# Kernel tuning notes

Hardware: AMD Instinct MI355X
Metric: run time of the kernel (lower is better)

The kernel has to match this reference:

```python
import jax, jax.numpy as jnp
import numpy as np

D_MODEL = 1024
D_FF = 4096


def _layernorm(x, g, b, eps=1e-5):
    mu = jnp.mean(x, axis=-1, keepdims=True)
    var = jnp.var(x, axis=-1, keepdims=True)
    return (x - mu) * jax.lax.rsqrt(var + eps) * g + b


def setup_inputs() -> dict:
    key = jax.random.key(0)
    ks = jax.random.split(key, 16)
    d, f = D_MODEL, D_FF
    s = 1.0 / np.sqrt(d)
    inp = {
        'x': jax.random.normal(ks[0], (4, 2048, d), dtype=jnp.float32),
        'wq': jax.random.uniform(ks[1], (d, d), jnp.float32, -s, s),
        'bq': jax.random.uniform(ks[2], (d,), jnp.float32, -s, s),
        'wk': jax.random.uniform(ks[3], (d, d), jnp.float32, -s, s),
        'bk': jax.random.uniform(ks[4], (d,), jnp.float32, -s, s),
        'wv': jax.random.uniform(ks[5], (d, d), jnp.float32, -s, s),
        'bv': jax.random.uniform(ks[6], (d,), jnp.float32, -s, s),
        'wo': jax.random.uniform(ks[7], (d, d), jnp.float32, -s, s),
        'bo': jax.random.uniform(ks[8], (d,), jnp.float32, -s, s),
        'w1': jax.random.uniform(ks[9], (d, f), jnp.float32, -s, s),
        'b1': jax.random.uniform(ks[10], (f,), jnp.float32, -s, s),
        'w2': jax.random.uniform(ks[11], (f, d), jnp.float32, -1.0 / np.sqrt(f), 1.0 / np.sqrt(f)),
        'b2': jax.random.uniform(ks[12], (d,), jnp.float32, -1.0 / np.sqrt(f), 1.0 / np.sqrt(f)),
        'g1': jnp.ones((d,), jnp.float32),
        'be1': jnp.zeros((d,), jnp.float32),
        'g2': jnp.ones((d,), jnp.float32),
        'be2': jnp.zeros((d,), jnp.float32),
    }
    return inp


def reference(x, wq, bq, wk, bk, wv, bv, wo, bo, w1, b1, w2, b2, g1, be1, g2, be2):
    d_k = x.shape[-1]
    q = jnp.einsum('bsd,de->bse', x, wq) + bq
    k = jnp.einsum('bsd,de->bse', x, wk) + bk
    v = jnp.einsum('bsd,de->bse', x, wv) + bv
    # full-width attention (no head split in the original module)
    scores = jnp.einsum('bqd,bkd->bqk', q, k) / jnp.sqrt(jnp.float32(d_k))
    attn = jax.nn.softmax(scores, axis=-1)
    ctx = jnp.einsum('bqk,bkd->bqd', attn, v)
    attn_out = jnp.einsum('bsd,de->bse', ctx, wo) + bo
    x1 = _layernorm(x + attn_out, g1, be1)
    ff = jnp.einsum('bsf,fd->bsd', jax.nn.relu(jnp.einsum('bsd,df->bsf', x1, w1) + b1), w2) + b2
    return _layernorm(x1 + ff, g2, be2)
```

## Files before the change

### kernel.cpp

```cpp
#include <hip/hip_runtime.h>
#include <stdint.h>


using f32x4 = __attribute__((ext_vector_type(4))) float;
using s16x8 = __attribute__((ext_vector_type(8))) short;

__device__ __forceinline__ ushort f2b(float f) {
    union { float f; uint32_t u; } v; v.f = f;
    uint32_t u = v.u;
    return (ushort)((u + 0x7fffu + ((u >> 16) & 1u)) >> 16);
}
__device__ __forceinline__ float b2f(ushort b) {
    union { uint32_t u; float f; } v; v.u = ((uint32_t)b) << 16;
    return v.f;
}
__device__ __forceinline__ float to_f(float f) { return f; }
__device__ __forceinline__ float to_f(ushort b) { return b2f(b); }

__device__ __forceinline__ void async_ld16(const ushort* g, ushort* l) {
    __builtin_amdgcn_global_load_lds(
        (const __attribute__((address_space(1))) void*)g,
        (__attribute__((address_space(3))) void*)l,
        16, 0, 0);
}

#define WAITCNT_VM4 0x0F74
#define WAITCNT_VM0 0x0F70


__global__ __launch_bounds__(256) void cast_f2b4(const float* __restrict__ src,
                                                 ushort* __restrict__ dst,
                                                 long long n4) {
    long long i = (long long)blockIdx.x * 256 + threadIdx.x;
    if (i >= n4) return;
    float4 f = ((const float4*)src)[i];
    ushort4 o;
    o.x = f2b(f.x); o.y = f2b(f.y); o.z = f2b(f.z); o.w = f2b(f.w);
    ((ushort4*)dst)[i] = o;
}


template <typename T>
__global__ __launch_bounds__(256) void transpose_to_bf16(const T* __restrict__ src,
                                                         ushort* __restrict__ dst,
                                                         int R, int C, int srcLd,
                                                         long long ss, long long ds) {
    __shared__ float tile[32][33];
    src += (long long)blockIdx.z * ss;
    dst += (long long)blockIdx.z * ds;
    const int c0 = blockIdx.x * 32;
    const int r0 = blockIdx.y * 32;
    const int tx = threadIdx.x, ty = threadIdx.y;
#pragma unroll
    for (int i = 0; i < 4; i++) {
        int r = r0 + ty + i * 8;
        tile[ty + i * 8][tx] = to_f(src[(long long)r * srcLd + c0 + tx]);
    }
    __syncthreads();
#pragma unroll
    for (int i = 0; i < 4; i++) {
        int r = c0 + ty + i * 8;
        dst[(long long)r * R + r0 + tx] = f2b(tile[tx][ty + i * 8]);
    }
}


#define BM 128
#define BN 128
#define BKK 32
#define TILE_ELEMS (BM * BKK)

template <int OUT_BF16, int RELU, int HAS_BIAS>
__global__ __launch_bounds__(256) void gemm_bt(const ushort* __restrict__ A,
                                               const ushort* __restrict__ BT,
                                               void* __restrict__ Cp,
                                               const float* __restrict__ bias,
                                               int N, int K, int kChunks, float scale,
                                               int lda, int ldb, int ldc,
                                               long long sA, long long sB, long long sC,
                                               long long sK) {
    __shared__ ushort As[2 * TILE_ELEMS];
    __shared__ ushort Bs[2 * TILE_ELEMS];

    const int tid = threadIdx.x;
    const int kIdx = blockIdx.z % kChunks;
    const int bz = blockIdx.z / kChunks;
    const int kLen = K / kChunks;
    const int kOff = kIdx * kLen;
    const ushort* Ab = A + (long long)bz * sA;
    const ushort* Bb = BT + (long long)bz * sB;

    const int W = gridDim.x, H = gridDim.y;
    const int b = blockIdx.y * W + blockIdx.x;
    const int Hp = H >> 3;
    const int xcd = b & 7;
    const int s = b >> 3;
    const int tn = s / Hp;
    const int tm = xcd * Hp + (s % Hp);

    const int lane = tid & 63;
    const int wave = tid >> 6;
    const int wm = (wave >> 1) * 64;
    const int wn = (wave & 1) * 64;
    const int quad = lane >> 4;
    const int l16 = lane & 15;

    const int srow = wave * 32 + (lane >> 2);
    const int scol = (lane & 3) * 8;
    const ushort* AgL = Ab + (long long)(tm * BM + srow) * lda + scol + kOff;
    const ushort* BgL = Bb + (long long)(tn * BN + srow) * ldb + scol + kOff;
    ushort* AsL = As + wave * 1024;
    ushort* BsL = Bs + wave * 1024;
    const long long rstepA = (long long)16 * lda;
    const long long rstepB = (long long)16 * ldb;

    f32x4 acc[4][4];
#pragma unroll
    for (int i = 0; i < 4; i++)
#pragma unroll
        for (int j = 0; j < 4; j++) acc[i][j] = (f32x4){0.f, 0.f, 0.f, 0.f};

    {
        async_ld16(AgL, AsL);
        async_ld16(AgL + rstepA, AsL + 512);
        async_ld16(BgL, BsL);
        async_ld16(BgL + rstepB, BsL + 512);
    }

    int p = 0;
    for (int k0 = 0; k0 < kLen; k0 += BKK) {
        if (k0 + BKK < kLen) {
            const int q = p ^ 1;
            async_ld16(AgL + (k0 + BKK), AsL + q * TILE_ELEMS);
            async_ld16(AgL + rstepA + (k0 + BKK), AsL + q * TILE_ELEMS + 512);
            async_ld16(BgL + (k0 + BKK), BsL + q * TILE_ELEMS);
            async_ld16(BgL + rstepB + (k0 + BKK), BsL + q * TILE_ELEMS + 512);
            __builtin_amdgcn_s_waitcnt(WAITCNT_VM4);
        } else {
            __builtin_amdgcn_s_waitcnt(WAITCNT_VM0);
        }
        __builtin_amdgcn_s_barrier();

        const ushort* Asp = As + p * TILE_ELEMS;
        const ushort* Bsp = Bs + p * TILE_ELEMS;
        s16x8 af[4], bf[4];
#pragma unroll
        for (int i = 0; i < 4; i++)
            af[i] = *(const s16x8*)&Asp[(wm + i * 16 + l16) * BKK + quad * 8];
#pragma unroll
        for (int j = 0; j < 4; j++)
            bf[j] = *(const s16x8*)&Bsp[(wn + j * 16 + l16) * BKK + quad * 8];
#pragma unroll
        for (int i = 0; i < 4; i++)
#pragma unroll
            for (int j = 0; j < 4; j++)
                acc[i][j] = __builtin_amdgcn_mfma_f32_16x16x32_bf16(af[i], bf[j], acc[i][j], 0, 0, 0);

        __builtin_amdgcn_s_barrier();
        p ^= 1;
    }

    const long long cb = (long long)bz * sC + (long long)kIdx * sK;
    float* Cf = (float*)Cp;
    ushort* Cb = (ushort*)Cp;
#pragma unroll
    for (int j = 0; j < 4; j++) {
        const int col = tn * BN + wn + j * 16 + l16;
        float bv = (HAS_BIAS && kIdx == 0) ? bias[col] : 0.0f;
#pragma unroll
        for (int i = 0; i < 4; i++) {
            const int row0 = tm * BM + wm + i * 16 + quad * 4;
#pragma unroll
            for (int r = 0; r < 4; r++) {
                float v = acc[i][j][r] * scale + bv;
                if (RELU) v = v > 0.f ? v : 0.f;
                long long idx = cb + (long long)(row0 + r) * ldc + col;
                if (OUT_BF16) Cb[idx] = f2b(v);
                else Cf[idx] = v;
            }
        }
    }
}


__global__ __launch_bounds__(256) void softmax_rows(const ushort* __restrict__ S,
                                                    ushort* __restrict__ P) {
    const int C = 2048;
    const long long row = blockIdx.x;
    const int tid = threadIdx.x;
    const ushort4* s4 = (const ushort4*)(S + row * C) + tid * 2;
    ushort4 a = s4[0], bq = s4[1];
    float v[8];
    v[0] = b2f(a.x); v[1] = b2f(a.y); v[2] = b2f(a.z); v[3] = b2f(a.w);
    v[4] = b2f(bq.x); v[5] = b2f(bq.y); v[6] = b2f(bq.z); v[7] = b2f(bq.w);
    float mx = -1e30f;
#pragma unroll
    for (int i = 0; i < 8; i++) mx = fmaxf(mx, v[i]);
    __shared__ float red[256];
    red[tid] = mx;
    __syncthreads();
    for (int off = 128; off > 0; off >>= 1) {
        if (tid < off) red[tid] = fmaxf(red[tid], red[tid + off]);
        __syncthreads();
    }
    mx = red[0];
    __syncthreads();
    float sum = 0.f;
#pragma unroll
    for (int i = 0; i < 8; i++) {
        v[i] = __expf(v[i] - mx);
        sum += v[i];
    }
    red[tid] = sum;
    __syncthreads();
    for (int off = 128; off > 0; off >>= 1) {
        if (tid < off) red[tid] += red[tid + off];
        __syncthreads();
    }
    float inv = 1.f / red[0];
    ushort4 o0, o1;
    o0.x = f2b(v[0] * inv); o0.y = f2b(v[1] * inv); o0.z = f2b(v[2] * inv); o0.w = f2b(v[3] * inv);
    o1.x = f2b(v[4] * inv); o1.y = f2b(v[5] * inv); o1.z = f2b(v[6] * inv); o1.w = f2b(v[7] * inv);
    ushort4* p4 = (ushort4*)(P + row * C) + tid * 2;
    p4[0] = o0;
    p4[1] = o1;
}


__global__ __launch_bounds__(256) void residual_ln(const float* __restrict__ X,
                                                   const float* __restrict__ Y,
                                                   const float* __restrict__ Y2,
                                                   const float* __restrict__ g,
                                                   const float* __restrict__ be,
                                                   float* __restrict__ outf,
                                                   ushort* __restrict__ outb) {
    const int D = 1024;
    const long long row = blockIdx.x;
    const float* x = X + row * D;
    const float* y = Y + row * D;
    const float* y2 = Y2 ? Y2 + row * D : nullptr;
    const int tid = threadIdx.x;
    float v[4];
    float s = 0.f, s2 = 0.f;
#pragma unroll
    for (int i = 0; i < 4; i++) {
        int c = tid + i * 256;
        float t = x[c] + y[c];
        if (y2) t += y2[c];
        v[i] = t;
        s += t;
        s2 += t * t;
    }
    __shared__ float r1[256], r2[256];
    r1[tid] = s;
    r2[tid] = s2;
    __syncthreads();
    for (int off = 128; off > 0; off >>= 1) {
        if (tid < off) {
            r1[tid] += r1[tid + off];
            r2[tid] += r2[tid + off];
        }
        __syncthreads();
    }
    float mu = r1[0] * (1.f / 1024.f);
    float var = r2[0] * (1.f / 1024.f) - mu * mu;
    float inv = rsqrtf(var + 1e-5f);
    float* of = outf + row * D;
    ushort* ob = outb ? outb + row * D : nullptr;
#pragma unroll
    for (int i = 0; i < 4; i++) {
        int c = tid + i * 256;
        float o = (v[i] - mu) * inv * g[c] + be[c];
        of[c] = o;
        if (ob) ob[c] = f2b(o);
    }
}


extern "C" void kernel_launch(void* const* d_in, const int* in_sizes, int n_in,
                              void* d_out, int out_size, void* d_ws, size_t ws_size,
                              hipStream_t stream) {
    const float* x  = (const float*)d_in[0];
    const float* wq = (const float*)d_in[1];
    const float* bq = (const float*)d_in[2];
    const float* wk = (const float*)d_in[3];
    const float* bk = (const float*)d_in[4];
    const float* wv = (const float*)d_in[5];
    const float* bv = (const float*)d_in[6];
    const float* wo = (const float*)d_in[7];
    const float* bo = (const float*)d_in[8];
    const float* w1 = (const float*)d_in[9];
    const float* b1 = (const float*)d_in[10];
    const float* w2 = (const float*)d_in[11];
    const float* b2 = (const float*)d_in[12];
    const float* g1 = (const float*)d_in[13];
    const float* be1 = (const float*)d_in[14];
    const float* g2 = (const float*)d_in[15];
    const float* be2 = (const float*)d_in[16];
    float* out = (float*)d_out;
    char* ws = (char*)d_ws;

    const int Bz = 4, S = 2048, D = 1024, F = 4096;
    const int T = Bz * S;
    const size_t MBy = 1024ull * 1024ull;

    ushort* qkvT = (ushort*)(ws + 0);
    ushort* woT  = (ushort*)(ws + 6 * MBy);
    ushort* w1T  = (ushort*)(ws + 8 * MBy);
    ushort* w2T  = (ushort*)(ws + 16 * MBy);
    float*  bqkv = (float*)(ws + 24 * MBy);
    ushort* xb   = (ushort*)(ws + 25 * MBy);
    ushort* qkv  = (ushort*)(ws + 41 * MBy);
    ushort* vT   = (ushort*)(ws + 89 * MBy);
    ushort* scb  = (ushort*)(ws + 105 * MBy);
    ushort* attn = (ushort*)(ws + 169 * MBy);
    ushort* ctx = (ushort*)(ws + 25 * MBy);
    float*  ao0 = (float*)(ws + 105 * MBy);
    float*  ao1 = (float*)(ws + 137 * MBy);
    float*  x1  = (float*)(ws + 41 * MBy);
    ushort* x1b = (ushort*)(ws + 73 * MBy);
    ushort* h   = (ushort*)(ws + 105 * MBy);
    float*  ff0 = (float*)(ws + 169 * MBy);
    float*  ff1 = (float*)(ws + 73 * MBy);

    dim3 b32(32, 8);

    cast_f2b4<<<(T * D) / 1024, 256, 0, stream>>>(x, xb, (long long)(T * D) / 4);

    transpose_to_bf16<float><<<dim3(32, 32, 1), b32, 0, stream>>>(wq, qkvT, D, D, D, 0, 0);
    transpose_to_bf16<float><<<dim3(32, 32, 1), b32, 0, stream>>>(wk, qkvT + 1024 * 1024, D, D, D, 0, 0);
    transpose_to_bf16<float><<<dim3(32, 32, 1), b32, 0, stream>>>(wv, qkvT + 2048 * 1024, D, D, D, 0, 0);
    transpose_to_bf16<float><<<dim3(32, 32, 1), b32, 0, stream>>>(wo, woT, D, D, D, 0, 0);
    transpose_to_bf16<float><<<dim3(128, 32, 1), b32, 0, stream>>>(w1, w1T, D, F, F, 0, 0);
    transpose_to_bf16<float><<<dim3(32, 128, 1), b32, 0, stream>>>(w2, w2T, F, D, D, 0, 0);

    hipMemcpyAsync(bqkv, bq, D * sizeof(float), hipMemcpyDeviceToDevice, stream);
    hipMemcpyAsync(bqkv + D, bk, D * sizeof(float), hipMemcpyDeviceToDevice, stream);
    hipMemcpyAsync(bqkv + 2 * D, bv, D * sizeof(float), hipMemcpyDeviceToDevice, stream);

    gemm_bt<1, 0, 1><<<dim3(3 * D / 128, T / 128, 1), 256, 0, stream>>>(
        xb, qkvT, qkv, bqkv, 3 * D, D, 1, 1.f, D, D, 3 * D, 0, 0, 0, 0);

    transpose_to_bf16<ushort><<<dim3(D / 32, S / 32, Bz), b32, 0, stream>>>(
        qkv + 2048, vT, S, D, 3 * D, (long long)S * 3 * D, (long long)S * D);

    gemm_bt<1, 0, 0><<<dim3(S / 128, S / 128, Bz), 256, 0, stream>>>(
        qkv, qkv + 1024, scb, nullptr, S, D, 1, 0.03125f, 3 * D, 3 * D, S,
        (long long)S * 3 * D, (long long)S * 3 * D, (long long)S * S, 0);

    softmax_rows<<<T, 256, 0, stream>>>(scb, attn);

    gemm_bt<1, 0, 0><<<dim3(D / 128, S / 128, Bz), 256, 0, stream>>>(
        attn, vT, ctx, nullptr, D, S, 1, 1.f, S, S, D,
        (long long)S * S, (long long)D * S, (long long)S * D, 0);

    gemm_bt<0, 0, 1><<<dim3(D / 128, T / 128, 2), 256, 0, stream>>>(
        ctx, woT, ao0, bo, D, D, 2, 1.f, D, D, D, 0, 0, 0, (long long)(ao1 - ao0));

    residual_ln<<<T, 256, 0, stream>>>(x, ao0, ao1, g1, be1, x1, x1b);

    gemm_bt<1, 1, 1><<<dim3(F / 128, T / 128, 1), 256, 0, stream>>>(
        x1b, w1T, h, b1, F, D, 1, 1.f, D, D, F, 0, 0, 0, 0);

    gemm_bt<0, 0, 1><<<dim3(D / 128, T / 128, 2), 256, 0, stream>>>(
        h, w2T, ff0, b2, D, F, 2, 1.f, F, F, D, 0, 0, 0, (long long)(ff1 - ff0));

    residual_ln<<<T, 256, 0, stream>>>(x1, ff0, ff1, g2, be2, out, nullptr);
}
```

Measured before the change: 630.5 us.

## Use triple-buffered LDS pipeline with two-tile prefetch depth in GEMM

The bf16 MFMA GEMM kernel moves from double to triple buffering of its A and B LDS tiles. It prefetches two K-tiles ahead and waits with a vmcnt of 8 instead of 4, so global-load latency has more time to overlap with compute. In exchange, LDS use grows from 32KB to 48KB per block, which may lower occupancy.

Result: no change. 626.8 us (-0.6%).

```diff
diff --git a/kernel.cpp b/kernel.cpp
--- a/kernel.cpp
+++ b/kernel.cpp
@@ -24,6 +24,7 @@
         16, 0, 0);
 }
 
+#define WAITCNT_VM8 0x0F78
 #define WAITCNT_VM4 0x0F74
 #define WAITCNT_VM0 0x0F70
 
@@ -79,8 +80,8 @@
                                                int lda, int ldb, int ldc,
                                                long long sA, long long sB, long long sC,
                                                long long sK) {
-    __shared__ ushort As[2 * TILE_ELEMS];
-    __shared__ ushort Bs[2 * TILE_ELEMS];
+    __shared__ ushort As[3 * TILE_ELEMS];
+    __shared__ ushort Bs[3 * TILE_ELEMS];
 
     const int tid = threadIdx.x;
     const int kIdx = blockIdx.z % kChunks;
@@ -120,29 +121,38 @@
 #pragma unroll
         for (int j = 0; j < 4; j++) acc[i][j] = (f32x4){0.f, 0.f, 0.f, 0.f};
 
-    {
-        async_ld16(AgL, AsL);
-        async_ld16(AgL + rstepA, AsL + 512);
-        async_ld16(BgL, BsL);
-        async_ld16(BgL + rstepB, BsL + 512);
-    }
-
-    int p = 0;
-    for (int k0 = 0; k0 < kLen; k0 += BKK) {
-        if (k0 + BKK < kLen) {
-            const int q = p ^ 1;
-            async_ld16(AgL + (k0 + BKK), AsL + q * TILE_ELEMS);
-            async_ld16(AgL + rstepA + (k0 + BKK), AsL + q * TILE_ELEMS + 512);
-            async_ld16(BgL + (k0 + BKK), BsL + q * TILE_ELEMS);
-            async_ld16(BgL + rstepB + (k0 + BKK), BsL + q * TILE_ELEMS + 512);
+    const int nIter = kLen / BKK;
+
+    async_ld16(AgL, AsL);
+    async_ld16(AgL + rstepA, AsL + 512);
+    async_ld16(BgL, BsL);
+    async_ld16(BgL + rstepB, BsL + 512);
+    if (nIter > 1) {
+        async_ld16(AgL + BKK, AsL + TILE_ELEMS);
+        async_ld16(AgL + rstepA + BKK, AsL + TILE_ELEMS + 512);
+        async_ld16(BgL + BKK, BsL + TILE_ELEMS);
+        async_ld16(BgL + rstepB + BKK, BsL + TILE_ELEMS + 512);
+    }
+
+    int cur = 0;
+    int wsl = 2;
+    for (int it = 0; it < nIter; it++) {
+        if (it + 2 < nIter) {
+            const int k2 = (it + 2) * BKK;
+            async_ld16(AgL + k2, AsL + wsl * TILE_ELEMS);
+            async_ld16(AgL + rstepA + k2, AsL + wsl * TILE_ELEMS + 512);
+            async_ld16(BgL + k2, BsL + wsl * TILE_ELEMS);
+            async_ld16(BgL + rstepB + k2, BsL + wsl * TILE_ELEMS + 512);
+            __builtin_amdgcn_s_waitcnt(WAITCNT_VM8);
+        } else if (it + 1 < nIter) {
             __builtin_amdgcn_s_waitcnt(WAITCNT_VM4);
         } else {
             __builtin_amdgcn_s_waitcnt(WAITCNT_VM0);
         }
         __builtin_amdgcn_s_barrier();
 
-        const ushort* Asp = As + p * TILE_ELEMS;
-        const ushort* Bsp = Bs + p * TILE_ELEMS;
+        const ushort* Asp = As + cur * TILE_ELEMS;
+        const ushort* Bsp = Bs + cur * TILE_ELEMS;
         s16x8 af[4], bf[4];
 #pragma unroll
         for (int i = 0; i < 4; i++)
@@ -157,7 +167,8 @@
                 acc[i][j] = __builtin_amdgcn_mfma_f32_16x16x32_bf16(af[i], bf[j], acc[i][j], 0, 0, 0);
 
         __builtin_amdgcn_s_barrier();
-        p ^= 1;
+        cur = cur + 1 == 3 ? 0 : cur + 1;
+        wsl = wsl + 1 == 3 ? 0 : wsl + 1;
     }
 
     const long long cb = (long long)bz * sC + (long long)kIdx * sK;
```
